# Optimization experiments

Measured on AMD Instinct MI355X. Metric: run time of the kernel, lower is better.

## Reference

```python
import jax, jax.numpy as jnp
import numpy as np

B, N, K, D, L = 8, 1024, 16, 256, 3  # batch, max_node_num, neighbor fan-in, g_hidden_dim, layers


def setup_inputs() -> dict:
    key = jax.random.key(0)
    ks = jax.random.split(key, 14)
    f32 = jnp.float32
    scale = 1.0 / np.sqrt(D).astype(np.float32)
    randn = lambda k, s: jax.random.normal(k, s, dtype=f32)
    lens = jax.random.randint(ks[12], (B,), N // 2, N + 1)
    node_mask = (jnp.arange(N)[None, :] < lens[:, None]).astype(f32)
    return {
        "h0": randn(ks[0], (B, N, D)),
        "c0": randn(ks[1], (B, N, D)),
        "x_in": randn(ks[2], (B, N, D)),
        "x_out": randn(ks[3], (B, N, D)),
        "W_in": randn(ks[4], (4, D, D)) * scale,   # gates stacked: [i, o, f, cell]
        "U_in": randn(ks[5], (4, D, D)) * scale,
        "W_out": randn(ks[6], (4, D, D)) * scale,
        "U_out": randn(ks[7], (4, D, D)) * scale,
        "b": jnp.zeros((4, D), dtype=f32),
        "in_mask": jax.random.randint(ks[8], (B, N, K), 0, 2).astype(f32),
        "out_mask": jax.random.randint(ks[9], (B, N, K), 0, 2).astype(f32),
        "node_mask": node_mask,
        "in_nodes": jax.random.randint(ks[10], (B, N, K), 0, N, dtype=jnp.int32),
        "out_nodes": jax.random.randint(ks[11], (B, N, K), 0, N, dtype=jnp.int32),
        "num_layers": L,
    }


def _gather_agg(h, idx, nb_mask, node_mask):
    # h: [B,N,D], idx: [B,N,K] -> masked sum of neighbor hidden states [B,N,D]
    nb = jax.vmap(lambda hb, ib: hb[ib])(h, idx)           # [B,N,K,D]
    agg = jnp.einsum('bnkd,bnk->bnd', nb, nb_mask)
    return agg * node_mask[..., None]


def reference(h0, c0, x_in, x_out, W_in, U_in, W_out, U_out, b,
              in_mask, out_mask, node_mask, in_nodes, out_nodes, num_layers):
    h, c = h0, c0
    nm = node_mask[..., None]
    for _ in range(num_layers):
        h_in = _gather_agg(h, in_nodes, in_mask, node_mask)
        h_out = _gather_agg(h, out_nodes, out_mask, node_mask)
        # pre-activation for all 4 gates at once: [4,B,N,D]
        pre = (jnp.einsum('bnd,gde->gbne', x_in, W_in)
               + jnp.einsum('bnd,gde->gbne', h_in, U_in)
               + jnp.einsum('bnd,gde->gbne', x_out, W_out)
               + jnp.einsum('bnd,gde->gbne', h_out, U_out)
               + b[:, None, None, :])
        i_g = jax.nn.sigmoid(pre[0])
        o_g = jax.nn.sigmoid(pre[1])
        f_g = jax.nn.sigmoid(pre[2])
        g = jnp.tanh(pre[3])
        c = (f_g * c + i_g * g) * nm
        h = o_g * jnp.tanh(c) * nm
    return h
```

## Files before the change

### kernel.cpp

```cpp
#include <hip/hip_runtime.h>
#include <hip/hip_bf16.h>
#include <cstdint>
#include <cstddef>

typedef __hip_bfloat16 bf16;
typedef _Float16 f16;
typedef __attribute__((ext_vector_type(4))) float f32x4;
typedef __attribute__((ext_vector_type(8))) _Float16 f16x8;
typedef __attribute__((ext_vector_type(4))) _Float16 f16x4;
typedef __attribute__((ext_vector_type(4))) unsigned short u16x4;

#define BB 8
#define NN 1024
#define KK 16
#define DD 256
#define MM (BB * NN)
#define GW 1024
#define NLAYER 3

__device__ __forceinline__ float ldf(const void* p, size_t i, int isf32) {
  return isf32 ? ((const float*)p)[i] : __bfloat162float(((const bf16*)p)[i]);
}

__device__ __forceinline__ f32x4 ldf4(const void* p, size_t vi, int isf32) {
  f32x4 r;
  if (isf32) {
    r = ((const f32x4*)p)[vi];
  } else {
    u16x4 u = ((const u16x4*)p)[vi];
#pragma unroll
    for (int q = 0; q < 4; q++) {
      union { unsigned u; float f; } c;
      c.u = ((unsigned)u[q]) << 16;
      r[q] = c.f;
    }
  }
  return r;
}

__device__ __forceinline__ void gload_lds16(const void* g, void* l) {
  __builtin_amdgcn_global_load_lds(
      (const __attribute__((address_space(1))) unsigned int*)g,
      (__attribute__((address_space(3))) unsigned int*)l, 16, 0, 0);
}

__device__ __forceinline__ int detect_isf32_wave(const void* W) {
  int lane = threadIdx.x & 63;
  unsigned short b = ((const unsigned short*)W)[2 * lane];
  int e = (b >> 7) & 0xFF;
  int sane = ((e >= 105 && e <= 130) || (b & 0x7FFF) == 0) ? 1 : 0;
  unsigned long long m = __ballot(sane);
  return (__popcll(m) > 32) ? 0 : 1;
}

struct Params {
  const void *h0, *c0, *x_in, *x_out, *W_in, *U_in, *W_out, *U_out, *bvec;
  const void *in_mask, *out_mask, *node_mask;
  const int *in_nodes, *out_nodes;
  float *biasI, *nmF, *inmF, *outmF;
  f16 *h_cur, *c_cur, *A_buf, *BT;
  void* outp;
};

#define PREP_VEC_TOTAL (256 + 2048 + 32768 + 32768 + 524288 + 524288)
#define PREP_BLOCKS (256 + (PREP_VEC_TOTAL + 255) / 256)
__global__ void prep_k(Params p) {
  __shared__ float tile[64][65];
  int isf32 = detect_isf32_wave(p.W_in);
  int b = blockIdx.x;
  int t = threadIdx.x;

  if (b < 256) {
    int bx = b & 3, by = (b >> 2) & 3, z = b >> 4;
    int g = z & 3, which = z >> 2;
    const void* src = (which == 0) ? p.W_in : (which == 1) ? p.W_out
                     : (which == 2) ? p.U_in : p.U_out;
    int colofs = which * 256;
    size_t gbase = (size_t)g * DD * DD;
    int tx = t & 63, ty = t >> 6;
    int d0 = bx * 64, e0 = by * 64;
#pragma unroll
    for (int r = 0; r < 64; r += 4)
      tile[ty + r][tx] = ldf(src, gbase + (size_t)(d0 + ty + r) * DD + e0 + tx, isf32);
    __syncthreads();
#pragma unroll
    for (int r = 0; r < 64; r += 4)
      p.BT[(size_t)(4 * (e0 + ty + r) + g) * 1024 + colofs + d0 + tx] = (f16)tile[tx][ty + r];
    return;
  }

  size_t i = (size_t)(b - 256) * 256 + t;
  const size_t V0 = 256;
  const size_t V1 = V0 + 2048;
  const size_t V2 = V1 + 32768;
  const size_t V3 = V2 + 32768;
  const size_t V4 = V3 + 524288;
  const size_t V5 = V4 + 524288;
  if (i < V0) {
    f32x4 r;
#pragma unroll
    for (int g = 0; g < 4; g++) r[g] = ldf(p.bvec, (size_t)g * 256 + i, isf32);
    ((f32x4*)p.biasI)[i] = r;
  } else if (i < V1) {
    ((f32x4*)p.nmF)[i - V0] = ldf4(p.node_mask, i - V0, isf32);
  } else if (i < V2) {
    ((f32x4*)p.inmF)[i - V1] = ldf4(p.in_mask, i - V1, isf32);
  } else if (i < V3) {
    ((f32x4*)p.outmF)[i - V2] = ldf4(p.out_mask, i - V2, isf32);
  } else if (i < V4) {
    size_t j = i - V3;
    f32x4 hv = ldf4(p.h0, j, isf32);
    f32x4 cv = ldf4(p.c0, j, isf32);
    f16x4 ho, co;
#pragma unroll
    for (int q = 0; q < 4; q++) { ho[q] = (f16)hv[q]; co[q] = (f16)cv[q]; }
    ((f16x4*)p.h_cur)[j] = ho;
    ((f16x4*)p.c_cur)[j] = co;
  } else if (i < V5) {
    size_t j = i - V4;
    size_t m = j >> 6, d4 = (j & 63) * 4;
    f32x4 xi = ldf4(p.x_in, j, isf32);
    f32x4 xo = ldf4(p.x_out, j, isf32);
    f16x4 a, bq;
#pragma unroll
    for (int q = 0; q < 4; q++) { a[q] = (f16)xi[q]; bq[q] = (f16)xo[q]; }
    *(f16x4*)(p.A_buf + m * 1024 + d4)       = a;
    *(f16x4*)(p.A_buf + m * 1024 + 256 + d4) = bq;
  }
}

__global__ void gather_k(Params p) {
  int wave = threadIdx.x >> 6;
  int lane = threadIdx.x & 63;
  int m = blockIdx.x * 4 + wave;
  int l5 = lane & 31, dir = lane >> 5;
  int myidx = 0; float mymask = 0.f;
  if (lane < 16)      { myidx = p.in_nodes[(size_t)m * KK + lane];
                        mymask = p.inmF[(size_t)m * KK + lane]; }
  else if (lane < 32) { myidx = p.out_nodes[(size_t)m * KK + lane - 16];
                        mymask = p.outmF[(size_t)m * KK + lane - 16]; }
  const f16* hb = p.h_cur + (size_t)(m >> 10) * NN * DD;
  float acc[8] = {};
#pragma unroll
  for (int k = 0; k < KK; k++) {
    int src = dir * 16 + k;
    int idxk = __shfl(myidx, src);
    float wk = __shfl(mymask, src);
    f16x8 v = *(const f16x8*)(hb + (size_t)idxk * DD + l5 * 8);
#pragma unroll
    for (int q = 0; q < 8; q++) acc[q] += wk * (float)v[q];
  }
  float nm = p.nmF[m];
  f16x8 o;
#pragma unroll
  for (int q = 0; q < 8; q++) o[q] = (f16)(acc[q] * nm);
  *(f16x8*)(p.A_buf + (size_t)m * 1024 + 512 + dir * 256 + l5 * 8) = o;
}

__global__ __launch_bounds__(256, 4)
void gemm_k(Params p, int last) {
  __shared__ char smem[24576];
  f16* As = (f16*)smem;
  f16* Bs = (f16*)(smem + 8192);
  float* tileF = (float*)smem;
  int isf32 = detect_isf32_wave(p.W_in);
  int t = threadIdx.x;
  int w = t >> 6, lane = t & 63;
  int row16 = lane & 15, kgrp = lane >> 4;
  int mBase = blockIdx.x * 64, nBase = blockIdx.y * 128;
  int aoff[2][4], boff[2][2];
#pragma unroll
  for (int sub = 0; sub < 2; sub++) {
    int ch = ((sub * 4 + kgrp) ^ (row16 & 7)) * 8;
#pragma unroll
    for (int i = 0; i < 4; i++) aoff[sub][i] = (row16 + 16 * i) * 64 + ch;
#pragma unroll
    for (int j = 0; j < 2; j++) boff[sub][j] = (w * 32 + 16 * j + row16) * 64 + ch;
  }
  int srow = t >> 3;
  int scol = ((t & 7) ^ (srow & 7)) * 8;
  const f16* ga0 = p.A_buf + (size_t)(mBase + srow) * 1024 + scol;
  const f16* gb0 = p.BT + (size_t)(nBase + srow) * 1024 + scol;
  f32x4 acc[4][2] = {};
  for (int kt = 0; kt < 1024; kt += 64) {
    const f16* ga = ga0 + kt;
    const f16* gb = gb0 + kt;
#pragma unroll
    for (int q = 0; q < 2; q++)
      gload_lds16(ga + (size_t)(32 * q) * 1024, As + q * 2048 + t * 8);
#pragma unroll
    for (int q = 0; q < 4; q++)
      gload_lds16(gb + (size_t)(32 * q) * 1024, Bs + q * 2048 + t * 8);
    __syncthreads();
#pragma unroll
    for (int sub = 0; sub < 2; sub++) {
      f16x8 af[4], bfr[2];
#pragma unroll
      for (int i = 0; i < 4; i++) af[i] = *(const f16x8*)(As + aoff[sub][i]);
#pragma unroll
      for (int j = 0; j < 2; j++) bfr[j] = *(const f16x8*)(Bs + boff[sub][j]);
#pragma unroll
      for (int i = 0; i < 4; i++)
#pragma unroll
        for (int j = 0; j < 2; j++)
          acc[i][j] = __builtin_amdgcn_mfma_f32_16x16x32_f16(af[i], bfr[j], acc[i][j], 0, 0, 0);
    }
    __syncthreads();
  }

#pragma unroll
  for (int pp = 0; pp < 2; pp++) {
    __syncthreads();
    if ((w >> 1) == pp) {
#pragma unroll
      for (int i = 0; i < 4; i++)
#pragma unroll
        for (int j = 0; j < 2; j++) {
          int cl = (w & 1) * 32 + 16 * j + row16;
#pragma unroll
          for (int r = 0; r < 4; r++) {
            int rr = 16 * i + 4 * kgrp + r;
            int ch = (cl >> 2) ^ (rr & 7);
            tileF[rr * 64 + ch * 4 + (cl & 3)] = acc[i][j][r];
          }
        }
    }
    __syncthreads();
    int el = t & 15;
    int nb = nBase + 64 * pp;
    int eb = nb >> 2;
    f32x4 bv4 = *(const f32x4*)(p.biasI + nb + el * 4);
#pragma unroll
    for (int rep = 0; rep < 4; rep++) {
      int ml = rep * 16 + (t >> 4);
      int gm = mBase + ml;
      f32x4 vals = *(const f32x4*)(tileF + ml * 64 + ((el ^ (ml & 7))) * 4);
      float nm = p.nmF[gm];
      size_t ci = (size_t)gm * DD + eb + el;
      float cold = (float)p.c_cur[ci];
      float p_i = vals[0] + bv4[0];
      float p_o = vals[1] + bv4[1];
      float p_f = vals[2] + bv4[2];
      float p_g = vals[3] + bv4[3];
      float ig = 1.f / (1.f + expf(-p_i));
      float og = 1.f / (1.f + expf(-p_o));
      float fg = 1.f / (1.f + expf(-p_f));
      float gg = tanhf(p_g);
      float cn = (fg * cold + ig * gg) * nm;
      float hn = og * tanhf(cn) * nm;
      p.c_cur[ci] = (f16)cn;
      p.h_cur[ci] = (f16)hn;
      if (last) {
        if (isf32) ((float*)p.outp)[ci] = hn;
        else       ((bf16*)p.outp)[ci] = __float2bfloat16(hn);
      }
    }
  }
}

extern "C" void kernel_launch(void* const* d_in, const int* in_sizes, int n_in,
                              void* d_out, int out_size, void* d_ws, size_t ws_size,
                              hipStream_t stream) {
  char* ws = (char*)d_ws;
  f16*   h_cur = (f16*)(ws + 256);
  f16*   c_cur = h_cur + (size_t)MM * DD;
  f16*   A_buf = c_cur + (size_t)MM * DD;
  f16*   BT    = A_buf + (size_t)MM * 1024;
  float* biasI = (float*)(BT + (size_t)1024 * 1024);
  float* nmF   = biasI + 1024;
  float* inmF  = nmF + MM;
  float* outmF = inmF + (size_t)MM * KK;

  Params p;
  p.h0 = d_in[0]; p.c0 = d_in[1]; p.x_in = d_in[2]; p.x_out = d_in[3];
  p.W_in = d_in[4]; p.U_in = d_in[5]; p.W_out = d_in[6]; p.U_out = d_in[7];
  p.bvec = d_in[8]; p.in_mask = d_in[9]; p.out_mask = d_in[10]; p.node_mask = d_in[11];
  p.in_nodes = (const int*)d_in[12]; p.out_nodes = (const int*)d_in[13];
  p.biasI = biasI; p.nmF = nmF; p.inmF = inmF; p.outmF = outmF;
  p.h_cur = h_cur; p.c_cur = c_cur; p.A_buf = A_buf; p.BT = BT;
  p.outp = d_out;

  prep_k<<<PREP_BLOCKS, 256, 0, stream>>>(p);
  for (int l = 0; l < NLAYER; l++) {
    gather_k<<<MM / 4, 256, 0, stream>>>(p);
    gemm_k<<<dim3(MM / 64, GW / 128), 256, 0, stream>>>(p, l == NLAYER - 1);
  }
}
```

Before: 226.7 us.

## Precompute layer-invariant input projections once and use fast exp2-based activations

```diff
diff --git a/kernel.cpp b/kernel.cpp
--- a/kernel.cpp
+++ b/kernel.cpp
@@ -15,7 +15,6 @@
 #define KK 16
 #define DD 256
 #define MM (BB * NN)
-#define GW 1024
 #define NLAYER 3
 
 __device__ __forceinline__ float ldf(const void* p, size_t i, int isf32) {
@@ -53,12 +52,23 @@
   return (__popcll(m) > 32) ? 0 : 1;
 }
 
+__device__ __forceinline__ float fsigmoid(float x) {
+  float a = fminf(fmaxf(-1.44269504f * x, -126.f), 126.f);
+  float e = __builtin_amdgcn_exp2f(a);
+  return __builtin_amdgcn_rcpf(1.f + e);
+}
+__device__ __forceinline__ float ftanh(float x) {
+  float a = fminf(fmaxf(2.88539008f * x, -126.f), 126.f);
+  float e = __builtin_amdgcn_exp2f(a);
+  return 1.f - 2.f * __builtin_amdgcn_rcpf(1.f + e);
+}
+
 struct Params {
   const void *h0, *c0, *x_in, *x_out, *W_in, *U_in, *W_out, *U_out, *bvec;
   const void *in_mask, *out_mask, *node_mask;
   const int *in_nodes, *out_nodes;
-  float *biasI, *nmF, *inmF, *outmF;
-  f16 *h_cur, *c_cur, *A_buf, *BT;
+  float *biasI, *nmF, *inmF, *outmF, *XW;
+  f16 *h_cur, *c_cur, *A_buf, *X_buf, *BT_W, *BT_U;
   void* outp;
 };
 
@@ -75,7 +85,8 @@
     int g = z & 3, which = z >> 2;
     const void* src = (which == 0) ? p.W_in : (which == 1) ? p.W_out
                      : (which == 2) ? p.U_in : p.U_out;
-    int colofs = which * 256;
+    f16* dst = (which < 2) ? p.BT_W : p.BT_U;
+    int colofs = (which & 1) * 256;
     size_t gbase = (size_t)g * DD * DD;
     int tx = t & 63, ty = t >> 6;
     int d0 = bx * 64, e0 = by * 64;
@@ -85,7 +96,7 @@
     __syncthreads();
 #pragma unroll
     for (int r = 0; r < 64; r += 4)
-      p.BT[(size_t)(4 * (e0 + ty + r) + g) * 1024 + colofs + d0 + tx] = (f16)tile[tx][ty + r];
+      dst[(size_t)(4 * (e0 + ty + r) + g) * 512 + colofs + d0 + tx] = (f16)tile[tx][ty + r];
     return;
   }
 
@@ -124,8 +135,8 @@
     f16x4 a, bq;
 #pragma unroll
     for (int q = 0; q < 4; q++) { a[q] = (f16)xi[q]; bq[q] = (f16)xo[q]; }
-    *(f16x4*)(p.A_buf + m * 1024 + d4)       = a;
-    *(f16x4*)(p.A_buf + m * 1024 + 256 + d4) = bq;
+    *(f16x4*)(p.X_buf + m * 512 + d4)       = a;
+    *(f16x4*)(p.X_buf + m * 512 + 256 + d4) = bq;
   }
 }
 
@@ -154,59 +165,95 @@
   f16x8 o;
 #pragma unroll
   for (int q = 0; q < 8; q++) o[q] = (f16)(acc[q] * nm);
-  *(f16x8*)(p.A_buf + (size_t)m * 1024 + 512 + dir * 256 + l5 * 8) = o;
+  *(f16x8*)(p.A_buf + (size_t)m * 512 + dir * 256 + l5 * 8) = o;
+}
+
+__device__ __forceinline__ void gemm_core(const f16* gA, const f16* gB, char* smem,
+                                          int t, int mBase, int nBase,
+                                          f32x4 (&acc)[4][2]) {
+  f16* As = (f16*)smem;
+  f16* Bs = (f16*)(smem + 8192);
+  int w = t >> 6, lane = t & 63;
+  int row16 = lane & 15, kgrp = lane >> 4;
+  int aoff[2][4], boff[2][2];
+#pragma unroll
+  for (int sub = 0; sub < 2; sub++) {
+    int ch = ((sub * 4 + kgrp) ^ (row16 & 7)) * 8;
+#pragma unroll
+    for (int i = 0; i < 4; i++) aoff[sub][i] = (row16 + 16 * i) * 64 + ch;
+#pragma unroll
+    for (int j = 0; j < 2; j++) boff[sub][j] = (w * 32 + 16 * j + row16) * 64 + ch;
+  }
+  int srow = t >> 3;
+  int scol = ((t & 7) ^ (srow & 7)) * 8;
+  const f16* ga0 = gA + (size_t)(mBase + srow) * 512 + scol;
+  const f16* gb0 = gB + (size_t)(nBase + srow) * 512 + scol;
+  for (int kt = 0; kt < 512; kt += 64) {
+    const f16* ga = ga0 + kt;
+    const f16* gb = gb0 + kt;
+#pragma unroll
+    for (int q = 0; q < 2; q++)
+      gload_lds16(ga + (size_t)(32 * q) * 512, As + q * 2048 + t * 8);
+#pragma unroll
+    for (int q = 0; q < 4; q++)
+      gload_lds16(gb + (size_t)(32 * q) * 512, Bs + q * 2048 + t * 8);
+    __syncthreads();
+#pragma unroll
+    for (int sub = 0; sub < 2; sub++) {
+      f16x8 af[4], bfr[2];
+#pragma unroll
+      for (int i = 0; i < 4; i++) af[i] = *(const f16x8*)(As + aoff[sub][i]);
+#pragma unroll
+      for (int j = 0; j < 2; j++) bfr[j] = *(const f16x8*)(Bs + boff[sub][j]);
+#pragma unroll
+      for (int i = 0; i < 4; i++)
+#pragma unroll
+        for (int j = 0; j < 2; j++)
+          acc[i][j] = __builtin_amdgcn_mfma_f32_16x16x32_f16(af[i], bfr[j], acc[i][j], 0, 0, 0);
+    }
+    __syncthreads();
+  }
+}
+
+__global__ __launch_bounds__(256, 4)
+void gemmx_k(Params p) {
+  __shared__ char smem[24576];
+  int t = threadIdx.x;
+  int w = t >> 6, lane = t & 63, row16 = lane & 15;
+  int mBase = blockIdx.x * 64, nBase = blockIdx.y * 128;
+  f32x4 acc[4][2] = {};
+  gemm_core(p.X_buf, p.BT_W, smem, t, mBase, nBase, acc);
+  float b0 = p.biasI[nBase + w * 32 + row16];
+  float b1 = p.biasI[nBase + w * 32 + 16 + row16];
+  f32x4* dst = (f32x4*)p.XW + ((size_t)(blockIdx.y * 128 + blockIdx.x) * 256 + t) * 8;
+#pragma unroll
+  for (int i = 0; i < 4; i++)
+#pragma unroll
+    for (int j = 0; j < 2; j++) {
+      f32x4 v = acc[i][j];
+      float bb = j ? b1 : b0;
+#pragma unroll
+      for (int r = 0; r < 4; r++) v[r] += bb;
+      dst[i * 2 + j] = v;
+    }
 }
 
 __global__ __launch_bounds__(256, 4)
 void gemm_k(Params p, int last) {
   __shared__ char smem[24576];
-  f16* As = (f16*)smem;
-  f16* Bs = (f16*)(smem + 8192);
   float* tileF = (float*)smem;
   int isf32 = detect_isf32_wave(p.W_in);
   int t = threadIdx.x;
   int w = t >> 6, lane = t & 63;
   int row16 = lane & 15, kgrp = lane >> 4;
   int mBase = blockIdx.x * 64, nBase = blockIdx.y * 128;
-  int aoff[2][4], boff[2][2];
-#pragma unroll
-  for (int sub = 0; sub < 2; sub++) {
-    int ch = ((sub * 4 + kgrp) ^ (row16 & 7)) * 8;
-#pragma unroll
-    for (int i = 0; i < 4; i++) aoff[sub][i] = (row16 + 16 * i) * 64 + ch;
-#pragma unroll
-    for (int j = 0; j < 2; j++) boff[sub][j] = (w * 32 + 16 * j + row16) * 64 + ch;
-  }
-  int srow = t >> 3;
-  int scol = ((t & 7) ^ (srow & 7)) * 8;
-  const f16* ga0 = p.A_buf + (size_t)(mBase + srow) * 1024 + scol;
-  const f16* gb0 = p.BT + (size_t)(nBase + srow) * 1024 + scol;
-  f32x4 acc[4][2] = {};
-  for (int kt = 0; kt < 1024; kt += 64) {
-    const f16* ga = ga0 + kt;
-    const f16* gb = gb0 + kt;
-#pragma unroll
-    for (int q = 0; q < 2; q++)
-      gload_lds16(ga + (size_t)(32 * q) * 1024, As + q * 2048 + t * 8);
-#pragma unroll
-    for (int q = 0; q < 4; q++)
-      gload_lds16(gb + (size_t)(32 * q) * 1024, Bs + q * 2048 + t * 8);
-    __syncthreads();
-#pragma unroll
-    for (int sub = 0; sub < 2; sub++) {
-      f16x8 af[4], bfr[2];
-#pragma unroll
-      for (int i = 0; i < 4; i++) af[i] = *(const f16x8*)(As + aoff[sub][i]);
-#pragma unroll
-      for (int j = 0; j < 2; j++) bfr[j] = *(const f16x8*)(Bs + boff[sub][j]);
-#pragma unroll
-      for (int i = 0; i < 4; i++)
-#pragma unroll
-        for (int j = 0; j < 2; j++)
-          acc[i][j] = __builtin_amdgcn_mfma_f32_16x16x32_f16(af[i], bfr[j], acc[i][j], 0, 0, 0);
-    }
-    __syncthreads();
-  }
+  f32x4 acc[4][2];
+  const f32x4* xw = (const f32x4*)p.XW + ((size_t)(blockIdx.y * 128 + blockIdx.x) * 256 + t) * 8;
+#pragma unroll
+  for (int i = 0; i < 4; i++)
+#pragma unroll
+    for (int j = 0; j < 2; j++) acc[i][j] = xw[i * 2 + j];
+  gemm_core(p.A_buf, p.BT_U, smem, t, mBase, nBase, acc);
 
 #pragma unroll
   for (int pp = 0; pp < 2; pp++) {
@@ -229,7 +276,6 @@
     int el = t & 15;
     int nb = nBase + 64 * pp;
     int eb = nb >> 2;
-    f32x4 bv4 = *(const f32x4*)(p.biasI + nb + el * 4);
 #pragma unroll
     for (int rep = 0; rep < 4; rep++) {
       int ml = rep * 16 + (t >> 4);
@@ -238,16 +284,12 @@
       float nm = p.nmF[gm];
       size_t ci = (size_t)gm * DD + eb + el;
       float cold = (float)p.c_cur[ci];
-      float p_i = vals[0] + bv4[0];
-      float p_o = vals[1] + bv4[1];
-      float p_f = vals[2] + bv4[2];
-      float p_g = vals[3] + bv4[3];
-      float ig = 1.f / (1.f + expf(-p_i));
-      float og = 1.f / (1.f + expf(-p_o));
-      float fg = 1.f / (1.f + expf(-p_f));
-      float gg = tanhf(p_g);
+      float ig = fsigmoid(vals[0]);
+      float og = fsigmoid(vals[1]);
+      float fg = fsigmoid(vals[2]);
+      float gg = ftanh(vals[3]);
       float cn = (fg * cold + ig * gg) * nm;
-      float hn = og * tanhf(cn) * nm;
+      float hn = og * ftanh(cn) * nm;
       p.c_cur[ci] = (f16)cn;
       p.h_cur[ci] = (f16)hn;
       if (last) {
@@ -265,8 +307,11 @@
   f16*   h_cur = (f16*)(ws + 256);
   f16*   c_cur = h_cur + (size_t)MM * DD;
   f16*   A_buf = c_cur + (size_t)MM * DD;
-  f16*   BT    = A_buf + (size_t)MM * 1024;
-  float* biasI = (float*)(BT + (size_t)1024 * 1024);
+  f16*   X_buf = A_buf + (size_t)MM * 512;
+  f16*   BT_W  = X_buf + (size_t)MM * 512;
+  f16*   BT_U  = BT_W + (size_t)1024 * 512;
+  float* XW    = (float*)(BT_U + (size_t)1024 * 512);
+  float* biasI = XW + (size_t)MM * 1024;
   float* nmF   = biasI + 1024;
   float* inmF  = nmF + MM;
   float* outmF = inmF + (size_t)MM * KK;
@@ -276,13 +321,15 @@
   p.W_in = d_in[4]; p.U_in = d_in[5]; p.W_out = d_in[6]; p.U_out = d_in[7];
   p.bvec = d_in[8]; p.in_mask = d_in[9]; p.out_mask = d_in[10]; p.node_mask = d_in[11];
   p.in_nodes = (const int*)d_in[12]; p.out_nodes = (const int*)d_in[13];
-  p.biasI = biasI; p.nmF = nmF; p.inmF = inmF; p.outmF = outmF;
-  p.h_cur = h_cur; p.c_cur = c_cur; p.A_buf = A_buf; p.BT = BT;
+  p.biasI = biasI; p.nmF = nmF; p.inmF = inmF; p.outmF = outmF; p.XW = XW;
+  p.h_cur = h_cur; p.c_cur = c_cur; p.A_buf = A_buf; p.X_buf = X_buf;
+  p.BT_W = BT_W; p.BT_U = BT_U;
   p.outp = d_out;
 
   prep_k<<<PREP_BLOCKS, 256, 0, stream>>>(p);
+  gemmx_k<<<dim3(MM / 64, 8), 256, 0, stream>>>(p);
   for (int l = 0; l < NLAYER; l++) {
     gather_k<<<MM / 4, 256, 0, stream>>>(p);
-    gemm_k<<<dim3(MM / 64, GW / 128), 256, 0, stream>>>(p, l == NLAYER - 1);
-  }
-}
+    gemm_k<<<dim3(MM / 64, 8), 256, 0, stream>>>(p, l == NLAYER - 1);
+  }
+}
```

Measured after the change: 223.6 us. No clear change (-1.4%).
